# Performance work log

Hardware: AMD Instinct MI355X
Metric: run time of the kernel (lower is better)

Reference implementation:

```python
import jax, jax.numpy as jnp
import numpy as np
import math

D_MODEL = 1024
N_HEADS = 16
D_K = D_MODEL // N_HEADS
THETA = 10000.0
B, S = 4, 2048


def setup_inputs() -> dict:
    key = jax.random.key(0)
    ks = jax.random.split(key, 5)
    std = math.sqrt(2.0 / (D_MODEL + D_MODEL))
    mk = lambda k: jax.random.normal(k, (D_MODEL, D_MODEL), jnp.float32) * std
    return {
        "x": jax.random.normal(ks[0], (B, S, D_MODEL), jnp.float32),
        "Wq": mk(ks[1]),
        "Wk": mk(ks[2]),
        "Wv": mk(ks[3]),
        "Wo": mk(ks[4]),
        "token_positions": jnp.arange(S, dtype=jnp.int32),
    }


def _rope(x, token_positions):
    # x: [B, H, S, d_k]; rotate adjacent pairs
    dk2 = x.shape[-1] // 2
    freqs = 1.0 / THETA ** (jnp.arange(0, x.shape[-1], 2, dtype=jnp.float32) / x.shape[-1])
    angles = token_positions.astype(jnp.float32)[:, None] * freqs[None, :]  # [S, dk2]
    cos, sin = jnp.cos(angles), jnp.sin(angles)
    xp = x.reshape(*x.shape[:-1], dk2, 2)
    x1, x2 = xp[..., 0], xp[..., 1]
    r1 = x1 * cos - x2 * sin
    r2 = x1 * sin + x2 * cos
    return jnp.stack([r1, r2], axis=-1).reshape(x.shape)


def reference(x, Wq, Wk, Wv, Wo, token_positions):
    seq_len = x.shape[-2]
    qkv_w = jnp.concatenate([Wq, Wk, Wv], axis=0)  # [3*d_model, d_model]
    qkv = x @ qkv_w.T  # [B, S, 3*d_model]
    q, k, v = jnp.split(qkv, 3, axis=-1)

    def heads(t):  # [B, S, H*dk] -> [B, H, S, dk]
        return t.reshape(*t.shape[:-1], N_HEADS, D_K).swapaxes(-3, -2)

    q, k, v = heads(q), heads(k), heads(v)
    q = _rope(q, token_positions)
    k = _rope(k, token_positions)

    scores = jnp.einsum("bhqd,bhkd->bhqk", q, k) / math.sqrt(D_K)
    causal = jnp.tril(jnp.ones((seq_len, seq_len), dtype=bool))
    scores = jnp.where(causal[None, None], scores, -jnp.inf)
    attn = jax.nn.softmax(scores, axis=-1)
    out = jnp.einsum("bhqk,bhkd->bhqd", attn, v)  # [B, H, S, dk]
    out = out.swapaxes(-3, -2).reshape(*x.shape[:-1], D_MODEL)
    return out @ Wo.T
```

## Files before the change

kernel.cpp:

```cpp
#include <hip/hip_runtime.h>
#include <hip/hip_bf16.h>


#define S_LEN 2048
#define NH 16
#define BATCH 4

typedef __bf16 bf16x8 __attribute__((ext_vector_type(8)));
typedef float f32x4 __attribute__((ext_vector_type(4)));
typedef float f32x16 __attribute__((ext_vector_type(16)));

__device__ __forceinline__ unsigned short f2bf(float f) {
  __bf16 h = (__bf16)f;
  return __builtin_bit_cast(unsigned short, h);
}
__device__ __forceinline__ float bf2f(unsigned short u) {
  return (float)__builtin_bit_cast(__bf16, u);
}

__global__ __launch_bounds__(256) void cast_bf16_kernel(const float* __restrict__ in,
                                                        unsigned short* __restrict__ out,
                                                        int n4) {
  int i = blockIdx.x * 256 + threadIdx.x;
  if (i < n4) {
    const float4 v = reinterpret_cast<const float4*>(in)[i];
    ushort4 o;
    o.x = f2bf(v.x); o.y = f2bf(v.y); o.z = f2bf(v.z); o.w = f2bf(v.w);
    reinterpret_cast<ushort4*>(out)[i] = o;
  }
}

__global__ __launch_bounds__(256) void cast_w_kernel(const float* __restrict__ Wq,
                                                     const float* __restrict__ Wk,
                                                     const float* __restrict__ Wv,
                                                     const float* __restrict__ Wo,
                                                     unsigned short* __restrict__ WQKV,
                                                     unsigned short* __restrict__ WOB) {
  int i = blockIdx.x * 256 + threadIdx.x;
  int which = i >> 18;
  int idx = i & 262143;
  const float* src = (which == 0) ? Wq : (which == 1) ? Wk : (which == 2) ? Wv : Wo;
  unsigned short* dst = (which < 3) ? (WQKV + ((size_t)which << 20)) : WOB;
  const float4 v = reinterpret_cast<const float4*>(src)[idx];
  ushort4 o;
  o.x = f2bf(v.x); o.y = f2bf(v.y); o.z = f2bf(v.z); o.w = f2bf(v.w);
  reinterpret_cast<ushort4*>(dst)[idx] = o;
}

__global__ __launch_bounds__(256) void trig_kernel(const int* __restrict__ pos,
                                                   float2* __restrict__ trig) {
  int idx = blockIdx.x * 256 + threadIdx.x;
  int s = idx >> 5, i = idx & 31;
  float freq = expf(-0.28782313662425575f * (float)i);
  float a = (float)pos[s] * freq;
  trig[idx] = make_float2(cosf(a), sinf(a));
}

template <int OUT_BF16>
__global__ __launch_bounds__(256) void gemm_bt_kernel(const unsigned short* __restrict__ A,
                                                      const unsigned short* __restrict__ B,
                                                      void* __restrict__ Cv,
                                                      int M, int N, int K) {
  __shared__ unsigned short As[128 * 32];
  __shared__ unsigned short Bs[128 * 32];
  const int tid = threadIdx.x;
  const int w = tid >> 6;
  const int l = tid & 63;

  const int nwg = gridDim.x * gridDim.y;
  const int bid = blockIdx.y * gridDim.x + blockIdx.x;
  const int cpx = nwg >> 3;
  const int swz = (bid & 7) * cpx + (bid >> 3);
  const int bxi = swz % gridDim.x;
  const int byi = swz / gridDim.x;

  const size_t bm = (size_t)byi * 128;
  const size_t bn = (size_t)bxi * 128;
  const int wr = (w >> 1) * 64;
  const int wc = (w & 1) * 64;

  f32x4 acc[4][4];
#pragma unroll
  for (int m = 0; m < 4; ++m)
#pragma unroll
    for (int n = 0; n < 4; ++n) acc[m][n] = (f32x4){0.f, 0.f, 0.f, 0.f};

  const int srow = w * 16 + (l >> 2);
  const int scol = (l & 3) * 8;
  const unsigned short* gA = A + (bm + srow) * K + scol;
  const unsigned short* gB = B + (bn + srow) * K + scol;
  unsigned short* lA = &As[(w * 16) * 32];
  unsigned short* lB = &Bs[(w * 16) * 32];

  const int ldm = l & 15;
  const int ldk = (l >> 4) * 8;

  for (int k0 = 0; k0 < K; k0 += 32) {
    __builtin_amdgcn_global_load_lds((const __attribute__((address_space(1))) void*)(gA + k0),
                                     (__attribute__((address_space(3))) void*)lA, 16, 0, 0);
    __builtin_amdgcn_global_load_lds((const __attribute__((address_space(1))) void*)(gA + (size_t)64 * K + k0),
                                     (__attribute__((address_space(3))) void*)(lA + 64 * 32), 16, 0, 0);
    __builtin_amdgcn_global_load_lds((const __attribute__((address_space(1))) void*)(gB + k0),
                                     (__attribute__((address_space(3))) void*)lB, 16, 0, 0);
    __builtin_amdgcn_global_load_lds((const __attribute__((address_space(1))) void*)(gB + (size_t)64 * K + k0),
                                     (__attribute__((address_space(3))) void*)(lB + 64 * 32), 16, 0, 0);
    __syncthreads();

    bf16x8 av[4], bv[4];
#pragma unroll
    for (int m = 0; m < 4; ++m)
      av[m] = *(const bf16x8*)&As[(wr + m * 16 + ldm) * 32 + ldk];
#pragma unroll
    for (int n = 0; n < 4; ++n)
      bv[n] = *(const bf16x8*)&Bs[(wc + n * 16 + ldm) * 32 + ldk];
#pragma unroll
    for (int m = 0; m < 4; ++m)
#pragma unroll
      for (int n = 0; n < 4; ++n)
        acc[m][n] = __builtin_amdgcn_mfma_f32_16x16x32_bf16(av[m], bv[n], acc[m][n], 0, 0, 0);
    __syncthreads();
  }

  const size_t crow0 = bm + wr + ((l >> 4) * 4);
  const int ccol0 = wc + ldm;
#pragma unroll
  for (int m = 0; m < 4; ++m)
#pragma unroll
    for (int n = 0; n < 4; ++n)
#pragma unroll
      for (int i = 0; i < 4; ++i) {
        size_t idx = (crow0 + m * 16 + i) * (size_t)N + bn + ccol0 + n * 16;
        if (OUT_BF16)
          ((unsigned short*)Cv)[idx] = f2bf(acc[m][n][i]);
        else
          ((float*)Cv)[idx] = acc[m][n][i];
      }
}

__global__ __launch_bounds__(256) void rope_qk_kernel(const unsigned short* __restrict__ qkv,
                                                      const float2* __restrict__ trig,
                                                      unsigned short* __restrict__ Qf,
                                                      unsigned short* __restrict__ Kf) {
  const int row = blockIdx.x;
  const int b = row >> 11, s = row & 2047;
#pragma unroll
  for (int pp = 0; pp < 2; ++pp) {
    const int p = pp * 256 + threadIdx.x;
    const int h = p >> 5;
    const int i = p & 31;
    const float2 cs = trig[(s << 5) + i];
    const size_t qoff = (size_t)row * 3072 + 2 * p;
    const size_t dsto = ((size_t)(b * NH + h) << 17) + (size_t)(s >> 5) * 2048 +
                        (i >> 3) * 512 + (((i >> 2) & 1) * 32 + (s & 31)) * 8 + (i & 3) * 2;

    ushort2 qp = *(const ushort2*)&qkv[qoff];
    float q0 = bf2f(qp.x), q1 = bf2f(qp.y);
    ushort2 qo;
    qo.x = f2bf((q0 * cs.x - q1 * cs.y) * 0.125f);
    qo.y = f2bf((q0 * cs.y + q1 * cs.x) * 0.125f);
    *(ushort2*)&Qf[dsto] = qo;

    ushort2 kp = *(const ushort2*)&qkv[qoff + 1024];
    float k0 = bf2f(kp.x), k1 = bf2f(kp.y);
    ushort2 ko;
    ko.x = f2bf(k0 * cs.x - k1 * cs.y);
    ko.y = f2bf(k0 * cs.y + k1 * cs.x);
    *(ushort2*)&Kf[dsto] = ko;
  }
}

__global__ __launch_bounds__(256) void v_transpose_kernel(const unsigned short* __restrict__ qkv,
                                                          unsigned short* __restrict__ Vf) {
  __shared__ unsigned short tile[64][65];
  const int st = blockIdx.x;
  const int bh = blockIdx.y;
  const int b = bh >> 4, h = bh & 15;
  const int c = threadIdx.x & 63;
  const int r0 = threadIdx.x >> 6;
#pragma unroll
  for (int pp = 0; pp < 16; ++pp) {
    int r = pp * 4 + r0;
    tile[r][c] = qkv[(size_t)(b * S_LEN + st * 64 + r) * 3072 + 2048 + h * 64 + c];
  }
  __syncthreads();
  const int s = st * 64 + c;
  const size_t sbase = ((size_t)bh << 17) + (size_t)(s >> 5) * 2048 +
                       ((s >> 4) & 1) * 512 + (((s >> 3) & 1) * 32) * 8 + (s & 7);
#pragma unroll
  for (int pp = 0; pp < 16; ++pp) {
    int d = pp * 4 + r0;
    Vf[sbase + (size_t)(d >> 5) * 1024 + (d & 31) * 8] = tile[c][d];
  }
}

__global__ __launch_bounds__(256) void attn_kernel(const unsigned short* __restrict__ Qf,
                                                   const unsigned short* __restrict__ Kf,
                                                   const unsigned short* __restrict__ Vf,
                                                   unsigned short* __restrict__ att) {
  __shared__ float comb[2][64][36];
  const int l = threadIdx.x & 63;
  const int w = threadIdx.x >> 6;
  const int lq = l & 31;
  const int hi = l >> 5;

  const int i = blockIdx.x;
  const int xcd = i & 7;
  const int r = i >> 3;
  const int hd = (xcd << 3) | (r & 7);
  const int rr = r >> 3;
  const int b = hd >> 4, h = hd & 15;

  const int p = w >> 1;
  const int s_half = w & 1;
  const int qt = p ? (63 - rr) : rr;

  const size_t headf = (size_t)(b * NH + h) << 17;
  const int q = qt * 32 + lq;

  bf16x8 qf[4];
  {
    const unsigned short* qp = Qf + headf + (size_t)qt * 2048 + l * 8;
#pragma unroll
    for (int m = 0; m < 4; ++m) qf[m] = *(const bf16x8*)(qp + m * 512);
  }
  float l_run = 0.f;
  f32x16 o0, o1;
#pragma unroll
  for (int i2 = 0; i2 < 16; ++i2) { o0[i2] = 0.f; o1[i2] = 0.f; }

  const unsigned short* kbase = Kf + headf + l * 8;
  const unsigned short* vbase = Vf + headf + l * 8;

  for (int nt = s_half; nt <= qt; nt += 2) {
    f32x16 s;
#pragma unroll
    for (int i2 = 0; i2 < 16; ++i2) s[i2] = 0.f;
    const unsigned short* kp = kbase + (size_t)nt * 2048;
#pragma unroll
    for (int m = 0; m < 4; ++m)
      s = __builtin_amdgcn_mfma_f32_32x32x16_bf16(*(const bf16x8*)(kp + m * 512), qf[m], s, 0, 0, 0);

    float pr[16];
    if (nt == qt) {
#pragma unroll
      for (int r2 = 0; r2 < 16; ++r2) {
        const int key = nt * 32 + (r2 & 3) + 8 * (r2 >> 2) + 4 * hi;
        pr[r2] = (key <= q) ? __expf(s[r2] - 4.0f) : 0.f;
      }
    } else {
#pragma unroll
      for (int r2 = 0; r2 < 16; ++r2) pr[r2] = __expf(s[r2] - 4.0f);
    }
#pragma unroll
    for (int r2 = 0; r2 < 16; ++r2) l_run += pr[r2];

    unsigned int pw[8];
#pragma unroll
    for (int t = 0; t < 8; ++t)
      asm("v_cvt_pk_bf16_f32 %0, %1, %2" : "=v"(pw[t]) : "v"(pr[2 * t]), "v"(pr[2 * t + 1]));
    auto r0 = __builtin_amdgcn_permlane32_swap(pw[0], pw[2], false, false);
    auto r1 = __builtin_amdgcn_permlane32_swap(pw[1], pw[3], false, false);
    auto r2 = __builtin_amdgcn_permlane32_swap(pw[4], pw[6], false, false);
    auto r3 = __builtin_amdgcn_permlane32_swap(pw[5], pw[7], false, false);
    union { unsigned int u[4]; bf16x8 v; } pb0, pb1;
    pb0.u[0] = r0[0]; pb0.u[1] = r1[0]; pb0.u[2] = r0[1]; pb0.u[3] = r1[1];
    pb1.u[0] = r2[0]; pb1.u[1] = r3[0]; pb1.u[2] = r2[1]; pb1.u[3] = r3[1];

    const unsigned short* vp = vbase + (size_t)nt * 2048;
    o0 = __builtin_amdgcn_mfma_f32_32x32x16_bf16(*(const bf16x8*)(vp), pb0.v, o0, 0, 0, 0);
    o0 = __builtin_amdgcn_mfma_f32_32x32x16_bf16(*(const bf16x8*)(vp + 512), pb1.v, o0, 0, 0, 0);
    o1 = __builtin_amdgcn_mfma_f32_32x32x16_bf16(*(const bf16x8*)(vp + 1024), pb0.v, o1, 0, 0, 0);
    o1 = __builtin_amdgcn_mfma_f32_32x32x16_bf16(*(const bf16x8*)(vp + 1536), pb1.v, o1, 0, 0, 0);
  }

  if (s_half) {
    float* dst = &comb[p][l][0];
#pragma unroll
    for (int jj = 0; jj < 4; ++jj) {
      *(f32x4*)(dst + 4 * jj) = (f32x4){o0[4 * jj], o0[4 * jj + 1], o0[4 * jj + 2], o0[4 * jj + 3]};
      *(f32x4*)(dst + 16 + 4 * jj) = (f32x4){o1[4 * jj], o1[4 * jj + 1], o1[4 * jj + 2], o1[4 * jj + 3]};
    }
    dst[32] = l_run;
  }
  __syncthreads();
  if (!s_half) {
    const float* src = &comb[p][l][0];
#pragma unroll
    for (int jj = 0; jj < 4; ++jj) {
      f32x4 a = *(const f32x4*)(src + 4 * jj);
      f32x4 c = *(const f32x4*)(src + 16 + 4 * jj);
#pragma unroll
      for (int t = 0; t < 4; ++t) { o0[4 * jj + t] += a[t]; o1[4 * jj + t] += c[t]; }
    }
    l_run += src[32];
    const float l_tot = l_run + __shfl_xor(l_run, 32, 64);
    const float inv = 1.f / l_tot;
    unsigned short* op = att + (size_t)(b * S_LEN + q) * 1024 + h * 64;
#pragma unroll
    for (int jj = 0; jj < 4; ++jj) {
      ushort4 v0, v1;
      v0.x = f2bf(o0[4 * jj + 0] * inv); v0.y = f2bf(o0[4 * jj + 1] * inv);
      v0.z = f2bf(o0[4 * jj + 2] * inv); v0.w = f2bf(o0[4 * jj + 3] * inv);
      *(ushort4*)(op + 8 * jj + 4 * hi) = v0;
      v1.x = f2bf(o1[4 * jj + 0] * inv); v1.y = f2bf(o1[4 * jj + 1] * inv);
      v1.z = f2bf(o1[4 * jj + 2] * inv); v1.w = f2bf(o1[4 * jj + 3] * inv);
      *(ushort4*)(op + 32 + 8 * jj + 4 * hi) = v1;
    }
  }
}

extern "C" void kernel_launch(void* const* d_in, const int* in_sizes, int n_in,
                              void* d_out, int out_size, void* d_ws, size_t ws_size,
                              hipStream_t stream) {
  const float* x  = (const float*)d_in[0];
  const float* Wq = (const float*)d_in[1];
  const float* Wk = (const float*)d_in[2];
  const float* Wv = (const float*)d_in[3];
  const float* Wo = (const float*)d_in[4];
  const int* pos  = (const int*)d_in[5];
  float* out = (float*)d_out;

  char* ws = (char*)d_ws;
  unsigned short* XB   = (unsigned short*)(ws + 0);
  unsigned short* WQKV = (unsigned short*)(ws + 16777216);
  unsigned short* WOB  = (unsigned short*)(ws + 23068672);
  unsigned short* QKV  = (unsigned short*)(ws + 25165824);
  unsigned short* QF   = (unsigned short*)(ws + 75497472);
  unsigned short* KF   = (unsigned short*)(ws + 92274688);
  unsigned short* VF   = (unsigned short*)(ws + 109051904);
  unsigned short* ATT  = (unsigned short*)(ws + 125829120);
  float2* TRIG         = (float2*)(ws + 142606336);

  cast_bf16_kernel<<<8192, 256, 0, stream>>>(x, XB, 2097152);
  cast_w_kernel<<<4096, 256, 0, stream>>>(Wq, Wk, Wv, Wo, WQKV, WOB);
  trig_kernel<<<256, 256, 0, stream>>>(pos, TRIG);

  gemm_bt_kernel<1><<<dim3(24, 64), 256, 0, stream>>>(XB, WQKV, QKV, 8192, 3072, 1024);

  rope_qk_kernel<<<8192, 256, 0, stream>>>(QKV, TRIG, QF, KF);
  v_transpose_kernel<<<dim3(32, 64), 256, 0, stream>>>(QKV, VF);

  attn_kernel<<<2048, 256, 0, stream>>>(QF, KF, VF, ATT);

  gemm_bt_kernel<0><<<dim3(8, 64), 256, 0, stream>>>(ATT, WOB, out, 8192, 1024, 1024);
}
```

Before: 307.5 us.

## Fuse RoPE and V transpose into QKV GEMM epilogue

The QKV projection GEMM epilogue now stages each accumulator tile through LDS and applies RoPE (plus the Q scale) directly. It writes Q, K and V straight into the fragment layouts the attention kernel expects. This removes the intermediate QKV buffer round trip and two separate kernel launches. The trig table is precomputed in the matching swizzled layout, and the epilogue gains LDS staging and more address arithmetic.

```diff
diff --git a/kernel.cpp b/kernel.cpp
--- a/kernel.cpp
+++ b/kernel.cpp
@@ -47,22 +47,29 @@
   reinterpret_cast<ushort4*>(dst)[idx] = o;
 }
 
-__global__ __launch_bounds__(256) void trig_kernel(const int* __restrict__ pos,
-                                                   float2* __restrict__ trig) {
+__global__ __launch_bounds__(256) void trigf_kernel(const int* __restrict__ pos,
+                                                    float* __restrict__ trigF) {
   int idx = blockIdx.x * 256 + threadIdx.x;
   int s = idx >> 5, i = idx & 31;
   float freq = expf(-0.28782313662425575f * (float)i);
   float a = (float)pos[s] * freq;
-  trig[idx] = make_float2(cosf(a), sinf(a));
-}
-
-template <int OUT_BF16>
+  int off = (s >> 5) * 2048 + (i >> 3) * 512 + ((((i >> 2) & 1) * 32) + (s & 31)) * 8 + 2 * (i & 3);
+  trigF[off] = cosf(a);
+  trigF[off + 1] = sinf(a);
+}
+
+template <int FUSED>
 __global__ __launch_bounds__(256) void gemm_bt_kernel(const unsigned short* __restrict__ A,
                                                       const unsigned short* __restrict__ B,
                                                       void* __restrict__ Cv,
-                                                      int M, int N, int K) {
-  __shared__ unsigned short As[128 * 32];
-  __shared__ unsigned short Bs[128 * 32];
+                                                      int M, int N, int K,
+                                                      const float* __restrict__ trigF,
+                                                      unsigned short* __restrict__ Qf,
+                                                      unsigned short* __restrict__ Kf,
+                                                      unsigned short* __restrict__ Vf) {
+  __shared__ unsigned short SMEM[8192];
+  unsigned short* As = SMEM;
+  unsigned short* Bs = SMEM + 4096;
   const int tid = threadIdx.x;
   const int w = tid >> 6;
   const int l = tid & 63;
@@ -93,7 +100,8 @@
   unsigned short* lB = &Bs[(w * 16) * 32];
 
   const int ldm = l & 15;
-  const int ldk = (l >> 4) * 8;
+  const int lg = l >> 4;
+  const int ldk = lg * 8;
 
   for (int k0 = 0; k0 < K; k0 += 32) {
     __builtin_amdgcn_global_load_lds((const __attribute__((address_space(1))) void*)(gA + k0),
@@ -121,75 +129,78 @@
     __syncthreads();
   }
 
-  const size_t crow0 = bm + wr + ((l >> 4) * 4);
-  const int ccol0 = wc + ldm;
-#pragma unroll
-  for (int m = 0; m < 4; ++m)
-#pragma unroll
-    for (int n = 0; n < 4; ++n)
-#pragma unroll
-      for (int i = 0; i < 4; ++i) {
-        size_t idx = (crow0 + m * 16 + i) * (size_t)N + bn + ccol0 + n * 16;
-        if (OUT_BF16)
-          ((unsigned short*)Cv)[idx] = f2bf(acc[m][n][i]);
-        else
+  if constexpr (!FUSED) {
+    const size_t crow0 = bm + wr + lg * 4;
+    const int ccol0 = wc + ldm;
+#pragma unroll
+    for (int m = 0; m < 4; ++m)
+#pragma unroll
+      for (int n = 0; n < 4; ++n)
+#pragma unroll
+        for (int i = 0; i < 4; ++i) {
+          size_t idx = (crow0 + m * 16 + i) * (size_t)N + bn + ccol0 + n * 16;
           ((float*)Cv)[idx] = acc[m][n][i];
+        }
+  } else {
+    const int cb = (int)bn + wc;
+    const int region = cb >> 10;
+    const int h = (cb & 1023) >> 6;
+    const int rowbase0 = (int)bm + wr;
+    const int bidx = rowbase0 >> 11;
+    const size_t headf = ((size_t)(bidx * NH + h)) << 17;
+    unsigned short* dst = (region == 0) ? Qf : (region == 1) ? Kf : Vf;
+    unsigned short* scr = &SMEM[w * 1536];
+    const float qsc = (region == 0) ? 0.125f : 1.0f;
+
+#pragma unroll
+    for (int m = 0; m < 4; ++m) {
+      const int rowbase = rowbase0 + m * 16;
+      const int st5 = (rowbase & 2047) >> 5;
+      if (region < 2) {
+#pragma unroll
+        for (int n = 0; n < 4; ++n)
+#pragma unroll
+          for (int i = 0; i < 4; ++i)
+            scr[(lg * 4 + i) * 72 + n * 16 + ldm] = f2bf(acc[m][n][i]);
+#pragma unroll
+        for (int t = 0; t < 2; ++t) {
+          const int f = l + t * 64;
+          const int fd = f >> 4;
+          const int sl = f & 15;
+          bf16x8 v = *(const bf16x8*)&scr[sl * 72 + fd * 8];
+          const size_t off = (size_t)st5 * 2048 + (fd >> 1) * 512 +
+                             (size_t)(((fd & 1) * 32) + ((m & 1) * 16 + sl)) * 8;
+          f32x4 t0 = *(const f32x4*)&trigF[off];
+          f32x4 t1 = *(const f32x4*)&trigF[off + 4];
+          bf16x8 ov;
+#pragma unroll
+          for (int j = 0; j < 4; ++j) {
+            const float c = (j < 2) ? t0[2 * j] : t1[2 * (j - 2)];
+            const float s_ = (j < 2) ? t0[2 * j + 1] : t1[2 * (j - 2) + 1];
+            const float x = (float)v[2 * j];
+            const float y = (float)v[2 * j + 1];
+            ov[2 * j] = (__bf16)((x * c - y * s_) * qsc);
+            ov[2 * j + 1] = (__bf16)((x * s_ + y * c) * qsc);
+          }
+          *(bf16x8*)(dst + headf + off) = ov;
+        }
+      } else {
+#pragma unroll
+        for (int n = 0; n < 4; ++n)
+#pragma unroll
+          for (int i = 0; i < 4; ++i)
+            scr[(n * 16 + ldm) * 24 + lg * 4 + i] = f2bf(acc[m][n][i]);
+#pragma unroll
+        for (int t = 0; t < 2; ++t) {
+          const int sh = t;
+          const int dd = l;
+          bf16x8 v = *(const bf16x8*)&scr[dd * 24 + sh * 8];
+          const size_t off = (size_t)st5 * 2048 + (dd >> 5) * 1024 + (m & 1) * 512 +
+                             (size_t)(sh * 32 + (dd & 31)) * 8;
+          *(bf16x8*)(dst + headf + off) = v;
+        }
       }
-}
-
-__global__ __launch_bounds__(256) void rope_qk_kernel(const unsigned short* __restrict__ qkv,
-                                                      const float2* __restrict__ trig,
-                                                      unsigned short* __restrict__ Qf,
-                                                      unsigned short* __restrict__ Kf) {
-  const int row = blockIdx.x;
-  const int b = row >> 11, s = row & 2047;
-#pragma unroll
-  for (int pp = 0; pp < 2; ++pp) {
-    const int p = pp * 256 + threadIdx.x;
-    const int h = p >> 5;
-    const int i = p & 31;
-    const float2 cs = trig[(s << 5) + i];
-    const size_t qoff = (size_t)row * 3072 + 2 * p;
-    const size_t dsto = ((size_t)(b * NH + h) << 17) + (size_t)(s >> 5) * 2048 +
-                        (i >> 3) * 512 + (((i >> 2) & 1) * 32 + (s & 31)) * 8 + (i & 3) * 2;
-
-    ushort2 qp = *(const ushort2*)&qkv[qoff];
-    float q0 = bf2f(qp.x), q1 = bf2f(qp.y);
-    ushort2 qo;
-    qo.x = f2bf((q0 * cs.x - q1 * cs.y) * 0.125f);
-    qo.y = f2bf((q0 * cs.y + q1 * cs.x) * 0.125f);
-    *(ushort2*)&Qf[dsto] = qo;
-
-    ushort2 kp = *(const ushort2*)&qkv[qoff + 1024];
-    float k0 = bf2f(kp.x), k1 = bf2f(kp.y);
-    ushort2 ko;
-    ko.x = f2bf(k0 * cs.x - k1 * cs.y);
-    ko.y = f2bf(k0 * cs.y + k1 * cs.x);
-    *(ushort2*)&Kf[dsto] = ko;
-  }
-}
-
-__global__ __launch_bounds__(256) void v_transpose_kernel(const unsigned short* __restrict__ qkv,
-                                                          unsigned short* __restrict__ Vf) {
-  __shared__ unsigned short tile[64][65];
-  const int st = blockIdx.x;
-  const int bh = blockIdx.y;
-  const int b = bh >> 4, h = bh & 15;
-  const int c = threadIdx.x & 63;
-  const int r0 = threadIdx.x >> 6;
-#pragma unroll
-  for (int pp = 0; pp < 16; ++pp) {
-    int r = pp * 4 + r0;
-    tile[r][c] = qkv[(size_t)(b * S_LEN + st * 64 + r) * 3072 + 2048 + h * 64 + c];
-  }
-  __syncthreads();
-  const int s = st * 64 + c;
-  const size_t sbase = ((size_t)bh << 17) + (size_t)(s >> 5) * 2048 +
-                       ((s >> 4) & 1) * 512 + (((s >> 3) & 1) * 32) * 8 + (s & 7);
-#pragma unroll
-  for (int pp = 0; pp < 16; ++pp) {
-    int d = pp * 4 + r0;
-    Vf[sbase + (size_t)(d >> 5) * 1024 + (d & 31) * 8] = tile[c][d];
+    }
   }
 }
 
@@ -324,23 +335,21 @@
   unsigned short* XB   = (unsigned short*)(ws + 0);
   unsigned short* WQKV = (unsigned short*)(ws + 16777216);
   unsigned short* WOB  = (unsigned short*)(ws + 23068672);
-  unsigned short* QKV  = (unsigned short*)(ws + 25165824);
   unsigned short* QF   = (unsigned short*)(ws + 75497472);
   unsigned short* KF   = (unsigned short*)(ws + 92274688);
   unsigned short* VF   = (unsigned short*)(ws + 109051904);
   unsigned short* ATT  = (unsigned short*)(ws + 125829120);
-  float2* TRIG         = (float2*)(ws + 142606336);
+  float* TRIGF         = (float*)(ws + 142606336);
 
   cast_bf16_kernel<<<8192, 256, 0, stream>>>(x, XB, 2097152);
   cast_w_kernel<<<4096, 256, 0, stream>>>(Wq, Wk, Wv, Wo, WQKV, WOB);
-  trig_kernel<<<256, 256, 0, stream>>>(pos, TRIG);
-
-  gemm_bt_kernel<1><<<dim3(24, 64), 256, 0, stream>>>(XB, WQKV, QKV, 8192, 3072, 1024);
-
-  rope_qk_kernel<<<8192, 256, 0, stream>>>(QKV, TRIG, QF, KF);
-  v_transpose_kernel<<<dim3(32, 64), 256, 0, stream>>>(QKV, VF);
+  trigf_kernel<<<256, 256, 0, stream>>>(pos, TRIGF);
+
+  gemm_bt_kernel<1><<<dim3(24, 64), 256, 0, stream>>>(XB, WQKV, nullptr, 8192, 3072, 1024,
+                                                      TRIGF, QF, KF, VF);
 
   attn_kernel<<<2048, 256, 0, stream>>>(QF, KF, VF, ATT);
 
-  gemm_bt_kernel<0><<<dim3(8, 64), 256, 0, stream>>>(ATT, WOB, out, 8192, 1024, 1024);
-}
+  gemm_bt_kernel<0><<<dim3(8, 64), 256, 0, stream>>>(ATT, WOB, out, 8192, 1024, 1024,
+                                                     nullptr, nullptr, nullptr, nullptr);
+}
```

Measured after the change: 275.9 us. -10.3%, faster.
